# Performance work log

Measured on AMD Instinct MI355X. Metric: run time of the kernel, lower is better.

Reference implementation:

```python
import jax, jax.numpy as jnp
import numpy as np

N_NODES = 50000
N_EDGES = 800000
IN_DIM = 128
HIDDEN = 128
NUM_CLASSES = 2
NUM_GRAPHS = 512


def _linear_params(key, fan_in, fan_out):
    # torch nn.Linear default init: U(-1/sqrt(fan_in), 1/sqrt(fan_in))
    k1, k2 = jax.random.split(key)
    bound = 1.0 / np.sqrt(fan_in)
    W = jax.random.uniform(k1, (fan_in, fan_out), jnp.float32, -bound, bound)
    b = jax.random.uniform(k2, (fan_out,), jnp.float32, -bound, bound)
    return W, b


def setup_inputs() -> dict:
    key = jax.random.key(0)
    ks = jax.random.split(key, 8)
    x = jax.random.normal(ks[0], (N_NODES, IN_DIM), jnp.float32)
    edge_index = jax.random.randint(ks[1], (2, N_EDGES), 0, N_NODES, jnp.int64)
    batch = jnp.sort(jax.random.randint(ks[2], (N_NODES,), 0, NUM_GRAPHS, jnp.int64))
    W1a, b1a = _linear_params(ks[3], IN_DIM, HIDDEN)
    W1b, b1b = _linear_params(ks[4], HIDDEN, HIDDEN)
    W2a, b2a = _linear_params(ks[5], HIDDEN, HIDDEN)
    W2b, b2b = _linear_params(ks[6], HIDDEN, HIDDEN)
    Wfc, bfc = _linear_params(ks[7], HIDDEN, NUM_CLASSES)
    return {"x": x, "edge_index": edge_index, "batch": batch,
            "W1a": W1a, "b1a": b1a, "W1b": W1b, "b1b": b1b,
            "W2a": W2a, "b2a": b2a, "W2b": W2b, "b2b": b2b,
            "Wfc": Wfc, "bfc": bfc}


def _gin_layer(x, src, dst, Wa, ba, Wb, bb):
    # GINConv (eps=0): h_i = MLP(x_i + sum_{j->i} x_j)
    agg = jax.ops.segment_sum(x[src], dst, num_segments=N_NODES)
    h = x + agg
    h = jax.nn.relu(h @ Wa + ba)
    h = h @ Wb + bb
    return jax.nn.relu(h)  # outer F.relu in forward; dropout is identity (eval)


def reference(x, edge_index, batch, W1a, b1a, W1b, b1b, W2a, b2a, W2b, b2b, Wfc, bfc):
    src, dst = edge_index[0], edge_index[1]
    h = _gin_layer(x, src, dst, W1a, b1a, W1b, b1b)
    h = _gin_layer(h, src, dst, W2a, b2a, W2b, b2b)
    # global mean pool per graph
    sums = jax.ops.segment_sum(h, batch, num_segments=NUM_GRAPHS)
    counts = jax.ops.segment_sum(jnp.ones((N_NODES,), h.dtype), batch, num_segments=NUM_GRAPHS)
    g_emb = sums / jnp.maximum(counts, 1.0)[:, None]
    return g_emb @ Wfc + bfc  # [NUM_GRAPHS, NUM_CLASSES]
```

## Files before the change

### kernel.cpp

```cpp
#include <hip/hip_runtime.h>

typedef unsigned short ushort_t;
typedef unsigned int uint_t;

typedef __bf16 bf16x8 __attribute__((ext_vector_type(8)));
typedef float f32x4 __attribute__((ext_vector_type(4)));

#define N_NODES 50000
#define N_EDGES 800000
#define DIM 128
#define NUM_GRAPHS 512
#define LDA 136

#define ELL_CAP 64

#define NBUCK 256
#define BUCK_SZ 196
#define FIFO_CAP 4096
#define A_CHUNK 2048
#define A_BLOCKS ((N_EDGES + A_CHUNK - 1) / A_CHUNK)

#define PREP_X_BLOCKS 6250
#define PREP_W_BLOCKS 256
#define PREP_B_BLOCKS 196
#define PREP_TOTAL (A_BLOCKS + PREP_X_BLOCKS + PREP_W_BLOCKS + PREP_B_BLOCKS + 1)

__device__ __forceinline__ float bf2f(ushort_t u) {
    return __uint_as_float(((uint_t)u) << 16);
}
__device__ __forceinline__ ushort_t f2bf(float f) {
    uint_t u = __float_as_uint(f);
    u = (u + 0x7FFF + ((u >> 16) & 1)) >> 16;
    return (ushort_t)u;
}
__device__ __forceinline__ bf16x8 as_bf16x8(uint4 v) {
    return __builtin_bit_cast(bf16x8, v);
}

__global__ void zero_detect_kernel(int* gcnt, const void* xraw,
                                   const void* eiraw, int* flags) {
    int i = threadIdx.x;
    if (i < NBUCK) gcnt[i] = 0;
    if (i == 0) {
        const ushort_t* u = (const ushort_t*)xraw;
        int extreme = 0;
        for (int k = 0; k < 128; ++k) {
            int e = (u[k] >> 7) & 0xFF;
            if (e >= 0xC0) extreme++;
        }
        flags[0] = (extreme > 8) ? 1 : 0;
        const int* p = (const int*)eiraw;
        int nonzero = 0;
        for (int k = 1; k < 64; k += 2) nonzero += (p[k] != 0);
        flags[1] = (nonzero == 0) ? 1 : 0;
    }
}

__global__ __launch_bounds__(256) void prep_all_kernel(
    const void* xraw, const void* braw, const void* eiraw,
    const void* W0, const void* W1, const void* W2, const void* W3,
    const void* pb1a, const void* pb1b, const void* pb2a, const void* pb2b,
    const void* pWfc, const void* pbfc, const int* __restrict__ flags,
    ushort_t* __restrict__ xout, ushort_t* __restrict__ wpout,
    int* __restrict__ batch32, float* __restrict__ params,
    int* __restrict__ gcnt, uint_t* __restrict__ fifo) {
    __shared__ int lcnt[NBUCK];
    __shared__ int lbase[NBUCK];
    int b = blockIdx.x;
    int tid = threadIdx.x;
    if (b < A_BLOCKS) {
        lcnt[tid] = 0;
        __syncthreads();
        const int* p = (const int*)eiraw;
        int i64 = flags[1];
        int base_e = b * A_CHUNK;
        int gk[8], rk[8];
        uint_t pk[8];
#pragma unroll
        for (int k = 0; k < 8; ++k) {
            int e = base_e + k * 256 + tid;
            int valid = e < N_EDGES;
            int s = 0, d = 0;
            if (valid) {
                if (i64) { s = p[2 * e]; d = p[2 * (N_EDGES + e)]; }
                else     { s = p[e];     d = p[N_EDGES + e]; }
            }
            int g = d / BUCK_SZ;
            gk[k] = valid ? g : -1;
            pk[k] = (uint_t)s | ((uint_t)(d - g * BUCK_SZ) << 16);
            rk[k] = valid ? atomicAdd(&lcnt[g], 1) : 0;
        }
        __syncthreads();
        lbase[tid] = atomicAdd(&gcnt[tid], lcnt[tid]);
        __syncthreads();
#pragma unroll
        for (int k = 0; k < 8; ++k) {
            if (gk[k] >= 0) {
                int pos = lbase[gk[k]] + rk[k];
                if (pos < FIFO_CAP)
                    fifo[(size_t)gk[k] * FIFO_CAP + pos] = pk[k];
            }
        }
    } else if (b < A_BLOCKS + PREP_X_BLOCKS) {
        if (flags[0]) {
            int i = (b - A_BLOCKS) * 256 + tid;
            if (i < N_NODES * DIM / 4) {
                float4 v = ((const float4*)xraw)[i];
                ushort4 o;
                o.x = f2bf(v.x); o.y = f2bf(v.y); o.z = f2bf(v.z); o.w = f2bf(v.w);
                ((ushort4*)xout)[i] = o;
            }
        }
    } else if (b < A_BLOCKS + PREP_X_BLOCKS + PREP_W_BLOCKS) {
        int gidx = (b - A_BLOCKS - PREP_X_BLOCKS) * 256 + tid;
        int which = gidx >> 14;
        const void* W = (which == 0) ? W0 : (which == 1) ? W1 : (which == 2) ? W2 : W3;
        int idx = gidx & 16383;
        int j = idx & 7;
        int L = (idx >> 3) & 63;
        int t = (idx >> 9) & 7;
        int s = idx >> 12;
        int k = s * 32 + (L >> 4) * 8 + j;
        int n = t * 16 + (L & 15);
        int off = k * DIM + n;
        wpout[gidx] = flags[0] ? f2bf(((const float*)W)[off]) : ((const ushort_t*)W)[off];
    } else if (b < A_BLOCKS + PREP_X_BLOCKS + PREP_W_BLOCKS + PREP_B_BLOCKS) {
        int i = (b - A_BLOCKS - PREP_X_BLOCKS - PREP_W_BLOCKS) * 256 + tid;
        if (i < N_NODES) {
            const int* p = (const int*)braw;
            batch32[i] = flags[1] ? p[2 * i] : p[i];
        }
    } else {
        for (int i = tid; i < 770; i += 256) {
            const void* srcp;
            int j;
            if (i < 128)      { srcp = pb1a; j = i; }
            else if (i < 256) { srcp = pb1b; j = i - 128; }
            else if (i < 384) { srcp = pb2a; j = i - 256; }
            else if (i < 512) { srcp = pb2b; j = i - 384; }
            else if (i < 768) { srcp = pWfc; j = i - 512; }
            else              { srcp = pbfc; j = i - 768; }
            params[i] = flags[0] ? ((const float*)srcp)[j] : bf2f(((const ushort_t*)srcp)[j]);
        }
    }
}

__global__ __launch_bounds__(256) void scatter_kernel(const uint_t* __restrict__ fifo,
                                                      const int* __restrict__ gcnt,
                                                      int* __restrict__ cnt,
                                                      ushort_t* __restrict__ ell,
                                                      float* __restrict__ gsum) {
    __shared__ int lcnt[BUCK_SZ];
    int b = blockIdx.x;
    int tid = threadIdx.x;
    gsum[b * 256 + tid] = 0.f;
    if (tid < BUCK_SZ) lcnt[tid] = 0;
    __syncthreads();
    int n = gcnt[b];
    if (n > FIFO_CAP) n = FIFO_CAP;
    const uint_t* f = fifo + (size_t)b * FIFO_CAP;
    int node0 = b * BUCK_SZ;
    for (int i = tid; i < n; i += 256) {
        uint_t e = f[i];
        int dl = (int)(e >> 16);
        int slot = atomicAdd(&lcnt[dl], 1);
        if (slot < ELL_CAP)
            ell[(size_t)(node0 + dl) * ELL_CAP + slot] = (ushort_t)(e & 0xFFFFu);
    }
    __syncthreads();
    if (tid < BUCK_SZ) {
        int node = node0 + tid;
        if (node < N_NODES) {
            int deg = lcnt[tid];
            cnt[node] = (deg > ELL_CAP) ? ELL_CAP : deg;
        }
    }
}

__global__ __launch_bounds__(256) void agg_kernel(const ushort_t* __restrict__ featA,
                                                  const void* __restrict__ featB,
                                                  const int* __restrict__ flags,
                                                  const int* __restrict__ deg,
                                                  const ushort_t* __restrict__ ell,
                                                  ushort_t* __restrict__ hout) {
    int n = blockIdx.x * 16 + (threadIdx.x >> 4);
    int lane = threadIdx.x & 15;
    if (n >= N_NODES) return;
    const ushort_t* feat = featA;
    if (flags && !flags[0]) feat = (const ushort_t*)featB;
    const uint4* fp = reinterpret_cast<const uint4*>(feat);
    uint4 v = fp[(size_t)n * 16 + lane];
    float a0 = bf2f((ushort_t)(v.x & 0xffff));
    float a1 = bf2f((ushort_t)(v.x >> 16));
    float a2 = bf2f((ushort_t)(v.y & 0xffff));
    float a3 = bf2f((ushort_t)(v.y >> 16));
    float a4 = bf2f((ushort_t)(v.z & 0xffff));
    float a5 = bf2f((ushort_t)(v.z >> 16));
    float a6 = bf2f((ushort_t)(v.w & 0xffff));
    float a7 = bf2f((ushort_t)(v.w >> 16));
    int e1 = deg[n];
    const uint4* __restrict__ rp4 = reinterpret_cast<const uint4*>(ell + (size_t)n * ELL_CAP);
    const ushort_t* __restrict__ row = ell + (size_t)n * ELL_CAP;
    int j = 0;
#define ACC8(V) \
    a0 += bf2f((ushort_t)((V).x & 0xffff)); a1 += bf2f((ushort_t)((V).x >> 16)); \
    a2 += bf2f((ushort_t)((V).y & 0xffff)); a3 += bf2f((ushort_t)((V).y >> 16)); \
    a4 += bf2f((ushort_t)((V).z & 0xffff)); a5 += bf2f((ushort_t)((V).z >> 16)); \
    a6 += bf2f((ushort_t)((V).w & 0xffff)); a7 += bf2f((ushort_t)((V).w >> 16));
    for (; j + 8 <= e1; j += 8) {
        uint4 ra = rp4[j >> 3];
        int s0 = (int)(ra.x & 0xffff), s1 = (int)(ra.x >> 16);
        int s2 = (int)(ra.y & 0xffff), s3 = (int)(ra.y >> 16);
        int s4 = (int)(ra.z & 0xffff), s5 = (int)(ra.z >> 16);
        int s6 = (int)(ra.w & 0xffff), s7 = (int)(ra.w >> 16);
        uint4 g0 = fp[(size_t)s0 * 16 + lane];
        uint4 g1 = fp[(size_t)s1 * 16 + lane];
        uint4 g2 = fp[(size_t)s2 * 16 + lane];
        uint4 g3 = fp[(size_t)s3 * 16 + lane];
        uint4 g4 = fp[(size_t)s4 * 16 + lane];
        uint4 g5 = fp[(size_t)s5 * 16 + lane];
        uint4 g6 = fp[(size_t)s6 * 16 + lane];
        uint4 g7 = fp[(size_t)s7 * 16 + lane];
        ACC8(g0) ACC8(g1) ACC8(g2) ACC8(g3)
        ACC8(g4) ACC8(g5) ACC8(g6) ACC8(g7)
    }
    if (j + 4 <= e1) {
        uint2 ra = *reinterpret_cast<const uint2*>(row + j);
        int s0 = (int)(ra.x & 0xffff), s1 = (int)(ra.x >> 16);
        int s2 = (int)(ra.y & 0xffff), s3 = (int)(ra.y >> 16);
        uint4 g0 = fp[(size_t)s0 * 16 + lane];
        uint4 g1 = fp[(size_t)s1 * 16 + lane];
        uint4 g2 = fp[(size_t)s2 * 16 + lane];
        uint4 g3 = fp[(size_t)s3 * 16 + lane];
        ACC8(g0) ACC8(g1) ACC8(g2) ACC8(g3)
        j += 4;
    }
    for (; j < e1; ++j) {
        int s = (int)row[j];
        uint4 g0 = fp[(size_t)s * 16 + lane];
        ACC8(g0)
    }
#undef ACC8
    uint4 o;
    o.x = (uint_t)f2bf(a0) | ((uint_t)f2bf(a1) << 16);
    o.y = (uint_t)f2bf(a2) | ((uint_t)f2bf(a3) << 16);
    o.z = (uint_t)f2bf(a4) | ((uint_t)f2bf(a5) << 16);
    o.w = (uint_t)f2bf(a6) | ((uint_t)f2bf(a7) << 16);
    reinterpret_cast<uint4*>(hout)[(size_t)n * 16 + lane] = o;
}

__global__ __launch_bounds__(256) void mlp_kernel(const ushort_t* __restrict__ hin,
                                                  const ushort_t* __restrict__ wpA,
                                                  const float* __restrict__ ba,
                                                  const ushort_t* __restrict__ wpB,
                                                  const float* __restrict__ bb,
                                                  ushort_t* __restrict__ hout) {
    __shared__ ushort_t As[64 * LDA];
    int tid = threadIdx.x;
    int wave = tid >> 6;
    int lane = tid & 63;
    int quad = lane >> 4;
    int cl = lane & 15;
    int row0 = blockIdx.x * 64;

    bf16x8 B1[2][4], B2[2][4];
#pragma unroll
    for (int ti = 0; ti < 2; ++ti) {
        int t = 2 * wave + ti;
#pragma unroll
        for (int s = 0; s < 4; ++s) {
            B1[ti][s] = as_bf16x8(reinterpret_cast<const uint4*>(wpA)[(s * 8 + t) * 64 + lane]);
            B2[ti][s] = as_bf16x8(reinterpret_cast<const uint4*>(wpB)[(s * 8 + t) * 64 + lane]);
        }
    }

    for (int i = tid; i < 64 * 16; i += 256) {
        int r = i >> 4, c8 = i & 15;
        uint4 v = make_uint4(0u, 0u, 0u, 0u);
        int gr = row0 + r;
        if (gr < N_NODES)
            v = reinterpret_cast<const uint4*>(hin + (size_t)gr * DIM)[c8];
        *reinterpret_cast<uint4*>(&As[r * LDA + c8 * 8]) = v;
    }
    __syncthreads();

    f32x4 acc[4][2];
#pragma unroll
    for (int m = 0; m < 4; ++m)
#pragma unroll
        for (int ti = 0; ti < 2; ++ti)
#pragma unroll
            for (int r = 0; r < 4; ++r) acc[m][ti][r] = 0.f;

#pragma unroll
    for (int s = 0; s < 4; ++s) {
#pragma unroll
        for (int m = 0; m < 4; ++m) {
            bf16x8 a = *reinterpret_cast<const bf16x8*>(&As[(m * 16 + cl) * LDA + s * 32 + quad * 8]);
#pragma unroll
            for (int ti = 0; ti < 2; ++ti)
                acc[m][ti] = __builtin_amdgcn_mfma_f32_16x16x32_bf16(a, B1[ti][s], acc[m][ti], 0, 0, 0);
        }
    }
    __syncthreads();

#pragma unroll
    for (int ti = 0; ti < 2; ++ti) {
        int col = 32 * wave + ti * 16 + cl;
        float bv = ba[col];
#pragma unroll
        for (int m = 0; m < 4; ++m)
#pragma unroll
            for (int r = 0; r < 4; ++r) {
                float v = acc[m][ti][r] + bv;
                As[(m * 16 + quad * 4 + r) * LDA + col] = f2bf(fmaxf(v, 0.f));
            }
    }
    __syncthreads();

#pragma unroll
    for (int m = 0; m < 4; ++m)
#pragma unroll
        for (int ti = 0; ti < 2; ++ti)
#pragma unroll
            for (int r = 0; r < 4; ++r) acc[m][ti][r] = 0.f;

#pragma unroll
    for (int s = 0; s < 4; ++s) {
#pragma unroll
        for (int m = 0; m < 4; ++m) {
            bf16x8 a = *reinterpret_cast<const bf16x8*>(&As[(m * 16 + cl) * LDA + s * 32 + quad * 8]);
#pragma unroll
            for (int ti = 0; ti < 2; ++ti)
                acc[m][ti] = __builtin_amdgcn_mfma_f32_16x16x32_bf16(a, B2[ti][s], acc[m][ti], 0, 0, 0);
        }
    }

#pragma unroll
    for (int ti = 0; ti < 2; ++ti) {
        int col = 32 * wave + ti * 16 + cl;
        float bv = bb[col];
#pragma unroll
        for (int m = 0; m < 4; ++m)
#pragma unroll
            for (int r = 0; r < 4; ++r) {
                int gr = row0 + m * 16 + quad * 4 + r;
                if (gr < N_NODES) {
                    float v = acc[m][ti][r] + bv;
                    hout[(size_t)gr * DIM + col] = f2bf(fmaxf(v, 0.f));
                }
            }
    }
}

__global__ __launch_bounds__(256) void mlp_pool_kernel(const ushort_t* __restrict__ hin,
                                                       const ushort_t* __restrict__ wpA,
                                                       const float* __restrict__ ba,
                                                       const ushort_t* __restrict__ wpB,
                                                       const float* __restrict__ bb,
                                                       const int* __restrict__ batch32,
                                                       float* __restrict__ gsum) {
    __shared__ ushort_t As[64 * LDA];
    int tid = threadIdx.x;
    int wave = tid >> 6;
    int lane = tid & 63;
    int quad = lane >> 4;
    int cl = lane & 15;
    int row0 = blockIdx.x * 64;

    bf16x8 B1[2][4], B2[2][4];
#pragma unroll
    for (int ti = 0; ti < 2; ++ti) {
        int t = 2 * wave + ti;
#pragma unroll
        for (int s = 0; s < 4; ++s) {
            B1[ti][s] = as_bf16x8(reinterpret_cast<const uint4*>(wpA)[(s * 8 + t) * 64 + lane]);
            B2[ti][s] = as_bf16x8(reinterpret_cast<const uint4*>(wpB)[(s * 8 + t) * 64 + lane]);
        }
    }

    for (int i = tid; i < 64 * 16; i += 256) {
        int r = i >> 4, c8 = i & 15;
        uint4 v = make_uint4(0u, 0u, 0u, 0u);
        int gr = row0 + r;
        if (gr < N_NODES)
            v = reinterpret_cast<const uint4*>(hin + (size_t)gr * DIM)[c8];
        *reinterpret_cast<uint4*>(&As[r * LDA + c8 * 8]) = v;
    }
    __syncthreads();

    f32x4 acc[4][2];
#pragma unroll
    for (int m = 0; m < 4; ++m)
#pragma unroll
        for (int ti = 0; ti < 2; ++ti)
#pragma unroll
            for (int r = 0; r < 4; ++r) acc[m][ti][r] = 0.f;

#pragma unroll
    for (int s = 0; s < 4; ++s) {
#pragma unroll
        for (int m = 0; m < 4; ++m) {
            bf16x8 a = *reinterpret_cast<const bf16x8*>(&As[(m * 16 + cl) * LDA + s * 32 + quad * 8]);
#pragma unroll
            for (int ti = 0; ti < 2; ++ti)
                acc[m][ti] = __builtin_amdgcn_mfma_f32_16x16x32_bf16(a, B1[ti][s], acc[m][ti], 0, 0, 0);
        }
    }
    __syncthreads();

#pragma unroll
    for (int ti = 0; ti < 2; ++ti) {
        int col = 32 * wave + ti * 16 + cl;
        float bv = ba[col];
#pragma unroll
        for (int m = 0; m < 4; ++m)
#pragma unroll
            for (int r = 0; r < 4; ++r) {
                float v = acc[m][ti][r] + bv;
                As[(m * 16 + quad * 4 + r) * LDA + col] = f2bf(fmaxf(v, 0.f));
            }
    }
    __syncthreads();

#pragma unroll
    for (int m = 0; m < 4; ++m)
#pragma unroll
        for (int ti = 0; ti < 2; ++ti)
#pragma unroll
            for (int r = 0; r < 4; ++r) acc[m][ti][r] = 0.f;

#pragma unroll
    for (int s = 0; s < 4; ++s) {
#pragma unroll
        for (int m = 0; m < 4; ++m) {
            bf16x8 a = *reinterpret_cast<const bf16x8*>(&As[(m * 16 + cl) * LDA + s * 32 + quad * 8]);
#pragma unroll
            for (int ti = 0; ti < 2; ++ti)
                acc[m][ti] = __builtin_amdgcn_mfma_f32_16x16x32_bf16(a, B2[ti][s], acc[m][ti], 0, 0, 0);
        }
    }
    __syncthreads();

#pragma unroll
    for (int ti = 0; ti < 2; ++ti) {
        int col = 32 * wave + ti * 16 + cl;
        float bv = bb[col];
#pragma unroll
        for (int m = 0; m < 4; ++m)
#pragma unroll
            for (int r = 0; r < 4; ++r) {
                float v = acc[m][ti][r] + bv;
                As[(m * 16 + quad * 4 + r) * LDA + col] = f2bf(fmaxf(v, 0.f));
            }
    }
    __syncthreads();

    int c = tid & 127;
    int rbase = (tid >> 7) * 32;
    float accp = 0.f;
    int curg = -1;
    for (int r = rbase; r < rbase + 32; ++r) {
        int gr = row0 + r;
        if (gr >= N_NODES) break;
        int g = batch32[gr];
        if (g != curg) {
            if (curg >= 0) atomicAdd(&gsum[curg * DIM + c], accp);
            curg = g;
            accp = 0.f;
        }
        accp += bf2f(As[r * LDA + c]);
    }
    if (curg >= 0) atomicAdd(&gsum[curg * DIM + c], accp);
}

__global__ __launch_bounds__(64) void fc_kernel(const float* __restrict__ gsum,
                                                const int* __restrict__ batch,
                                                const float* __restrict__ params,
                                                const int* __restrict__ flags,
                                                void* __restrict__ out) {
    int g = blockIdx.x;
    int l = threadIdx.x;
    int lo = 0, hi = N_NODES;
    while (lo < hi) { int mid = (lo + hi) >> 1; if (batch[mid] < g) lo = mid + 1; else hi = mid; }
    int start = lo;
    hi = N_NODES;
    while (lo < hi) { int mid = (lo + hi) >> 1; if (batch[mid] < g + 1) lo = mid + 1; else hi = mid; }
    int cnt = lo - start;
    float inv = 1.0f / (float)(cnt > 0 ? cnt : 1);
    float m0 = gsum[g * DIM + l] * inv;
    float m1 = gsum[g * DIM + 64 + l] * inv;
    float p0 = m0 * params[512 + l * 2 + 0] + m1 * params[512 + (64 + l) * 2 + 0];
    float p1 = m0 * params[512 + l * 2 + 1] + m1 * params[512 + (64 + l) * 2 + 1];
#pragma unroll
    for (int off = 32; off > 0; off >>= 1) {
        p0 += __shfl_down(p0, off, 64);
        p1 += __shfl_down(p1, off, 64);
    }
    if (l == 0) {
        float o0 = p0 + params[768];
        float o1 = p1 + params[769];
        if (flags[0]) {
            ((float*)out)[g * 2 + 0] = o0;
            ((float*)out)[g * 2 + 1] = o1;
        } else {
            ((ushort_t*)out)[g * 2 + 0] = f2bf(o0);
            ((ushort_t*)out)[g * 2 + 1] = f2bf(o1);
        }
    }
}

extern "C" void kernel_launch(void* const* d_in, const int* in_sizes, int n_in,
                              void* d_out, int out_size, void* d_ws, size_t ws_size,
                              hipStream_t stream) {
    const void* x = d_in[0];
    const void* ei = d_in[1];
    const void* batch = d_in[2];
    const void* W1a = d_in[3];
    const void* b1a = d_in[4];
    const void* W1b = d_in[5];
    const void* b1b = d_in[6];
    const void* W2a = d_in[7];
    const void* b2a = d_in[8];
    const void* W2b = d_in[9];
    const void* b2b = d_in[10];
    const void* Wfc = d_in[11];
    const void* bfc = d_in[12];

    char* base = (char*)d_ws;
    ushort_t* hX = (ushort_t*)base;   base += (size_t)N_NODES * DIM * 2;
    ushort_t* hA = (ushort_t*)base;   base += (size_t)N_NODES * DIM * 2;
    ushort_t* ell = (ushort_t*)base;  base += (size_t)N_NODES * ELL_CAP * 2;
    uint_t* fifo = (uint_t*)base;     base += (size_t)NBUCK * FIFO_CAP * 4;
    int* cnt = (int*)base;            base += (size_t)N_NODES * 4;
    int* batch32 = (int*)base;        base += (size_t)N_NODES * 4;
    int* gcnt = (int*)base;           base += NBUCK * 4;
    ushort_t* wp = (ushort_t*)base;   base += 4 * 16384 * 2;
    float* params = (float*)base;     base += 772 * 4;
    float* gsum = (float*)base;       base += (size_t)NUM_GRAPHS * DIM * 4;
    int* flags = (int*)base;          base += 16;

    ushort_t* wpA1 = wp;
    ushort_t* wpB1 = wp + 16384;
    ushort_t* wpA2 = wp + 2 * 16384;
    ushort_t* wpB2 = wp + 3 * 16384;

    zero_detect_kernel<<<1, 256, 0, stream>>>(gcnt, x, ei, flags);
    prep_all_kernel<<<PREP_TOTAL, 256, 0, stream>>>(x, batch, ei, W1a, W1b, W2a, W2b,
                                                    b1a, b1b, b2a, b2b, Wfc, bfc, flags,
                                                    hX, wp, batch32, params, gcnt, fifo);
    scatter_kernel<<<NBUCK, 256, 0, stream>>>(fifo, gcnt, cnt, ell, gsum);

    agg_kernel<<<(N_NODES + 15) / 16, 256, 0, stream>>>(hX, x, flags, cnt, ell, hA);
    mlp_kernel<<<(N_NODES + 63) / 64, 256, 0, stream>>>(hA, wpA1, params + 0, wpB1, params + 128, hA);
    agg_kernel<<<(N_NODES + 15) / 16, 256, 0, stream>>>(hA, hA, nullptr, cnt, ell, hX);
    mlp_pool_kernel<<<(N_NODES + 63) / 64, 256, 0, stream>>>(hX, wpA2, params + 256, wpB2, params + 384,
                                                             batch32, gsum);
    fc_kernel<<<NUM_GRAPHS, 64, 0, stream>>>(gsum, batch32, params, flags, d_out);
}
```

Before: 226.9 us.

## Fuse GIN pipeline into a single cooperative persistent kernel with grid syncs

Replaces the chain of eight kernel launches with one cooperative persistent kernel that loops over virtual blocks for each stage and separates stages with grid-wide syncs. Flag detection moves into each block, which skips the x-conversion blocks when x is already bf16. Zeroing of gsum and gcnt moves to a memset, and the MLP now loads the second weight set after the first GEMM to lower register pressure. This removes launch gaps and inter-kernel drain, but grid.sync costs and a persistent grid capped at 1536 blocks may hurt load balance in the irregular aggregation stages.

```diff
diff --git a/kernel.cpp b/kernel.cpp
--- a/kernel.cpp
+++ b/kernel.cpp
@@ -1,4 +1,7 @@
 #include <hip/hip_runtime.h>
+#include <hip/hip_cooperative_groups.h>
+
+namespace cg = cooperative_groups;
 
 typedef unsigned short ushort_t;
 typedef unsigned int uint_t;
@@ -25,6 +28,12 @@
 #define PREP_B_BLOCKS 196
 #define PREP_TOTAL (A_BLOCKS + PREP_X_BLOCKS + PREP_W_BLOCKS + PREP_B_BLOCKS + 1)
 
+#define AGG_VBLOCKS ((N_NODES + 15) / 16)
+#define MLP_VBLOCKS ((N_NODES + 63) / 64)
+#define FC_VBLOCKS (NUM_GRAPHS / 4)
+
+#define SMEM_BYTES (64 * LDA * 2)
+
 __device__ __forceinline__ float bf2f(ushort_t u) {
     return __uint_as_float(((uint_t)u) << 16);
 }
@@ -37,42 +46,35 @@
     return __builtin_bit_cast(bf16x8, v);
 }
 
-__global__ void zero_detect_kernel(int* gcnt, const void* xraw,
-                                   const void* eiraw, int* flags) {
-    int i = threadIdx.x;
-    if (i < NBUCK) gcnt[i] = 0;
-    if (i == 0) {
-        const ushort_t* u = (const ushort_t*)xraw;
-        int extreme = 0;
-        for (int k = 0; k < 128; ++k) {
-            int e = (u[k] >> 7) & 0xFF;
-            if (e >= 0xC0) extreme++;
-        }
-        flags[0] = (extreme > 8) ? 1 : 0;
-        const int* p = (const int*)eiraw;
-        int nonzero = 0;
-        for (int k = 1; k < 64; k += 2) nonzero += (p[k] != 0);
-        flags[1] = (nonzero == 0) ? 1 : 0;
-    }
-}
-
-__global__ __launch_bounds__(256) void prep_all_kernel(
+__device__ __forceinline__ void detect_flags(const void* xraw, const void* eiraw,
+                                             int* f32f, int* i64f) {
+    const ushort_t* u = (const ushort_t*)xraw;
+    int extreme = 0;
+    for (int k = 0; k < 128; ++k) {
+        int e = (u[k] >> 7) & 0xFF;
+        if (e >= 0xC0) extreme++;
+    }
+    *f32f = (extreme > 8) ? 1 : 0;
+    const int* p = (const int*)eiraw;
+    int nonzero = 0;
+    for (int k = 1; k < 64; k += 2) nonzero += (p[k] != 0);
+    *i64f = (nonzero == 0) ? 1 : 0;
+}
+
+__device__ __forceinline__ void dev_prep(
+    int b, int tid, char* smemc,
     const void* xraw, const void* braw, const void* eiraw,
     const void* W0, const void* W1, const void* W2, const void* W3,
     const void* pb1a, const void* pb1b, const void* pb2a, const void* pb2b,
-    const void* pWfc, const void* pbfc, const int* __restrict__ flags,
-    ushort_t* __restrict__ xout, ushort_t* __restrict__ wpout,
-    int* __restrict__ batch32, float* __restrict__ params,
-    int* __restrict__ gcnt, uint_t* __restrict__ fifo) {
-    __shared__ int lcnt[NBUCK];
-    __shared__ int lbase[NBUCK];
-    int b = blockIdx.x;
-    int tid = threadIdx.x;
+    const void* pWfc, const void* pbfc, int f32f, int i64f, int xblocks,
+    ushort_t* xout, ushort_t* wpout, int* batch32, float* params,
+    int* gcnt, uint_t* fifo) {
+    int* lcnt = (int*)smemc;
+    int* lbase = lcnt + NBUCK;
     if (b < A_BLOCKS) {
         lcnt[tid] = 0;
         __syncthreads();
         const int* p = (const int*)eiraw;
-        int i64 = flags[1];
         int base_e = b * A_CHUNK;
         int gk[8], rk[8];
         uint_t pk[8];
@@ -82,8 +84,8 @@
             int valid = e < N_EDGES;
             int s = 0, d = 0;
             if (valid) {
-                if (i64) { s = p[2 * e]; d = p[2 * (N_EDGES + e)]; }
-                else     { s = p[e];     d = p[N_EDGES + e]; }
+                if (i64f) { s = p[2 * e]; d = p[2 * (N_EDGES + e)]; }
+                else      { s = p[e];     d = p[N_EDGES + e]; }
             }
             int g = d / BUCK_SZ;
             gk[k] = valid ? g : -1;
@@ -101,8 +103,8 @@
                     fifo[(size_t)gk[k] * FIFO_CAP + pos] = pk[k];
             }
         }
-    } else if (b < A_BLOCKS + PREP_X_BLOCKS) {
-        if (flags[0]) {
+    } else if (b < A_BLOCKS + xblocks) {
+        if (f32f) {
             int i = (b - A_BLOCKS) * 256 + tid;
             if (i < N_NODES * DIM / 4) {
                 float4 v = ((const float4*)xraw)[i];
@@ -111,8 +113,8 @@
                 ((ushort4*)xout)[i] = o;
             }
         }
-    } else if (b < A_BLOCKS + PREP_X_BLOCKS + PREP_W_BLOCKS) {
-        int gidx = (b - A_BLOCKS - PREP_X_BLOCKS) * 256 + tid;
+    } else if (b < A_BLOCKS + xblocks + PREP_W_BLOCKS) {
+        int gidx = (b - A_BLOCKS - xblocks) * 256 + tid;
         int which = gidx >> 14;
         const void* W = (which == 0) ? W0 : (which == 1) ? W1 : (which == 2) ? W2 : W3;
         int idx = gidx & 16383;
@@ -123,12 +125,12 @@
         int k = s * 32 + (L >> 4) * 8 + j;
         int n = t * 16 + (L & 15);
         int off = k * DIM + n;
-        wpout[gidx] = flags[0] ? f2bf(((const float*)W)[off]) : ((const ushort_t*)W)[off];
-    } else if (b < A_BLOCKS + PREP_X_BLOCKS + PREP_W_BLOCKS + PREP_B_BLOCKS) {
-        int i = (b - A_BLOCKS - PREP_X_BLOCKS - PREP_W_BLOCKS) * 256 + tid;
+        wpout[gidx] = f32f ? f2bf(((const float*)W)[off]) : ((const ushort_t*)W)[off];
+    } else if (b < A_BLOCKS + xblocks + PREP_W_BLOCKS + PREP_B_BLOCKS) {
+        int i = (b - A_BLOCKS - xblocks - PREP_W_BLOCKS) * 256 + tid;
         if (i < N_NODES) {
             const int* p = (const int*)braw;
-            batch32[i] = flags[1] ? p[2 * i] : p[i];
+            batch32[i] = i64f ? p[2 * i] : p[i];
         }
     } else {
         for (int i = tid; i < 770; i += 256) {
@@ -140,20 +142,15 @@
             else if (i < 512) { srcp = pb2b; j = i - 384; }
             else if (i < 768) { srcp = pWfc; j = i - 512; }
             else              { srcp = pbfc; j = i - 768; }
-            params[i] = flags[0] ? ((const float*)srcp)[j] : bf2f(((const ushort_t*)srcp)[j]);
-        }
-    }
-}
-
-__global__ __launch_bounds__(256) void scatter_kernel(const uint_t* __restrict__ fifo,
-                                                      const int* __restrict__ gcnt,
-                                                      int* __restrict__ cnt,
-                                                      ushort_t* __restrict__ ell,
-                                                      float* __restrict__ gsum) {
-    __shared__ int lcnt[BUCK_SZ];
-    int b = blockIdx.x;
-    int tid = threadIdx.x;
-    gsum[b * 256 + tid] = 0.f;
+            params[i] = f32f ? ((const float*)srcp)[j] : bf2f(((const ushort_t*)srcp)[j]);
+        }
+    }
+}
+
+__device__ __forceinline__ void dev_scatter(int b, int tid, char* smemc,
+                                            const uint_t* fifo, const int* gcnt,
+                                            int* cnt, ushort_t* ell) {
+    int* lcnt = (int*)smemc;
     if (tid < BUCK_SZ) lcnt[tid] = 0;
     __syncthreads();
     int n = gcnt[b];
@@ -177,17 +174,12 @@
     }
 }
 
-__global__ __launch_bounds__(256) void agg_kernel(const ushort_t* __restrict__ featA,
-                                                  const void* __restrict__ featB,
-                                                  const int* __restrict__ flags,
-                                                  const int* __restrict__ deg,
-                                                  const ushort_t* __restrict__ ell,
-                                                  ushort_t* __restrict__ hout) {
-    int n = blockIdx.x * 16 + (threadIdx.x >> 4);
-    int lane = threadIdx.x & 15;
+__device__ __forceinline__ void dev_agg(int b, int tid, const ushort_t* feat,
+                                        const int* deg, const ushort_t* ell,
+                                        ushort_t* hout) {
+    int n = b * 16 + (tid >> 4);
+    int lane = tid & 15;
     if (n >= N_NODES) return;
-    const ushort_t* feat = featA;
-    if (flags && !flags[0]) feat = (const ushort_t*)featB;
     const uint4* fp = reinterpret_cast<const uint4*>(feat);
     uint4 v = fp[(size_t)n * 16 + lane];
     float a0 = bf2f((ushort_t)(v.x & 0xffff));
@@ -199,8 +191,8 @@
     float a6 = bf2f((ushort_t)(v.w & 0xffff));
     float a7 = bf2f((ushort_t)(v.w >> 16));
     int e1 = deg[n];
-    const uint4* __restrict__ rp4 = reinterpret_cast<const uint4*>(ell + (size_t)n * ELL_CAP);
-    const ushort_t* __restrict__ row = ell + (size_t)n * ELL_CAP;
+    const uint4* rp4 = reinterpret_cast<const uint4*>(ell + (size_t)n * ELL_CAP);
+    const ushort_t* row = ell + (size_t)n * ELL_CAP;
     int j = 0;
 #define ACC8(V) \
     a0 += bf2f((ushort_t)((V).x & 0xffff)); a1 += bf2f((ushort_t)((V).x >> 16)); \
@@ -249,31 +241,21 @@
     reinterpret_cast<uint4*>(hout)[(size_t)n * 16 + lane] = o;
 }
 
-__global__ __launch_bounds__(256) void mlp_kernel(const ushort_t* __restrict__ hin,
-                                                  const ushort_t* __restrict__ wpA,
-                                                  const float* __restrict__ ba,
-                                                  const ushort_t* __restrict__ wpB,
-                                                  const float* __restrict__ bb,
-                                                  ushort_t* __restrict__ hout) {
-    __shared__ ushort_t As[64 * LDA];
-    int tid = threadIdx.x;
-    int wave = tid >> 6;
-    int lane = tid & 63;
-    int quad = lane >> 4;
-    int cl = lane & 15;
-    int row0 = blockIdx.x * 64;
-
-    bf16x8 B1[2][4], B2[2][4];
+__device__ __forceinline__ void dev_mlp(int b, int tid, char* smemc,
+                                        const ushort_t* hin, const ushort_t* wpA,
+                                        const float* ba, const ushort_t* wpB,
+                                        const float* bb, ushort_t* hout) {
+    ushort_t* As = (ushort_t*)smemc;
+    int wave = tid >> 6, lane = tid & 63, quad = lane >> 4, cl = lane & 15;
+    int row0 = b * 64;
+    bf16x8 B[2][4];
 #pragma unroll
     for (int ti = 0; ti < 2; ++ti) {
         int t = 2 * wave + ti;
 #pragma unroll
-        for (int s = 0; s < 4; ++s) {
-            B1[ti][s] = as_bf16x8(reinterpret_cast<const uint4*>(wpA)[(s * 8 + t) * 64 + lane]);
-            B2[ti][s] = as_bf16x8(reinterpret_cast<const uint4*>(wpB)[(s * 8 + t) * 64 + lane]);
-        }
-    }
-
+        for (int s = 0; s < 4; ++s)
+            B[ti][s] = as_bf16x8(reinterpret_cast<const uint4*>(wpA)[(s * 8 + t) * 64 + lane]);
+    }
     for (int i = tid; i < 64 * 16; i += 256) {
         int r = i >> 4, c8 = i & 15;
         uint4 v = make_uint4(0u, 0u, 0u, 0u);
@@ -283,7 +265,6 @@
         *reinterpret_cast<uint4*>(&As[r * LDA + c8 * 8]) = v;
     }
     __syncthreads();
-
     f32x4 acc[4][2];
 #pragma unroll
     for (int m = 0; m < 4; ++m)
@@ -291,19 +272,16 @@
         for (int ti = 0; ti < 2; ++ti)
 #pragma unroll
             for (int r = 0; r < 4; ++r) acc[m][ti][r] = 0.f;
-
-#pragma unroll
-    for (int s = 0; s < 4; ++s) {
+#pragma unroll
+    for (int s = 0; s < 4; ++s)
 #pragma unroll
         for (int m = 0; m < 4; ++m) {
             bf16x8 a = *reinterpret_cast<const bf16x8*>(&As[(m * 16 + cl) * LDA + s * 32 + quad * 8]);
 #pragma unroll
             for (int ti = 0; ti < 2; ++ti)
-                acc[m][ti] = __builtin_amdgcn_mfma_f32_16x16x32_bf16(a, B1[ti][s], acc[m][ti], 0, 0, 0);
-        }
-    }
-    __syncthreads();
-
+                acc[m][ti] = __builtin_amdgcn_mfma_f32_16x16x32_bf16(a, B[ti][s], acc[m][ti], 0, 0, 0);
+        }
+    __syncthreads();
 #pragma unroll
     for (int ti = 0; ti < 2; ++ti) {
         int col = 32 * wave + ti * 16 + cl;
@@ -317,25 +295,28 @@
             }
     }
     __syncthreads();
-
+#pragma unroll
+    for (int ti = 0; ti < 2; ++ti) {
+        int t = 2 * wave + ti;
+#pragma unroll
+        for (int s = 0; s < 4; ++s)
+            B[ti][s] = as_bf16x8(reinterpret_cast<const uint4*>(wpB)[(s * 8 + t) * 64 + lane]);
+    }
 #pragma unroll
     for (int m = 0; m < 4; ++m)
 #pragma unroll
         for (int ti = 0; ti < 2; ++ti)
 #pragma unroll
             for (int r = 0; r < 4; ++r) acc[m][ti][r] = 0.f;
-
-#pragma unroll
-    for (int s = 0; s < 4; ++s) {
+#pragma unroll
+    for (int s = 0; s < 4; ++s)
 #pragma unroll
         for (int m = 0; m < 4; ++m) {
             bf16x8 a = *reinterpret_cast<const bf16x8*>(&As[(m * 16 + cl) * LDA + s * 32 + quad * 8]);
 #pragma unroll
             for (int ti = 0; ti < 2; ++ti)
-                acc[m][ti] = __builtin_amdgcn_mfma_f32_16x16x32_bf16(a, B2[ti][s], acc[m][ti], 0, 0, 0);
-        }
-    }
-
+                acc[m][ti] = __builtin_amdgcn_mfma_f32_16x16x32_bf16(a, B[ti][s], acc[m][ti], 0, 0, 0);
+        }
 #pragma unroll
     for (int ti = 0; ti < 2; ++ti) {
         int col = 32 * wave + ti * 16 + cl;
@@ -351,34 +332,25 @@
                 }
             }
     }
-}
-
-__global__ __launch_bounds__(256) void mlp_pool_kernel(const ushort_t* __restrict__ hin,
-                                                       const ushort_t* __restrict__ wpA,
-                                                       const float* __restrict__ ba,
-                                                       const ushort_t* __restrict__ wpB,
-                                                       const float* __restrict__ bb,
-                                                       const int* __restrict__ batch32,
-                                                       float* __restrict__ gsum) {
-    __shared__ ushort_t As[64 * LDA];
-    int tid = threadIdx.x;
-    int wave = tid >> 6;
-    int lane = tid & 63;
-    int quad = lane >> 4;
-    int cl = lane & 15;
-    int row0 = blockIdx.x * 64;
-
-    bf16x8 B1[2][4], B2[2][4];
+    __syncthreads();
+}
+
+__device__ __forceinline__ void dev_mlp_pool(int b, int tid, char* smemc,
+                                             const ushort_t* hin, const ushort_t* wpA,
+                                             const float* ba, const ushort_t* wpB,
+                                             const float* bb, const int* batch32,
+                                             float* gsum) {
+    ushort_t* As = (ushort_t*)smemc;
+    int wave = tid >> 6, lane = tid & 63, quad = lane >> 4, cl = lane & 15;
+    int row0 = b * 64;
+    bf16x8 B[2][4];
 #pragma unroll
     for (int ti = 0; ti < 2; ++ti) {
         int t = 2 * wave + ti;
 #pragma unroll
-        for (int s = 0; s < 4; ++s) {
-            B1[ti][s] = as_bf16x8(reinterpret_cast<const uint4*>(wpA)[(s * 8 + t) * 64 + lane]);
-            B2[ti][s] = as_bf16x8(reinterpret_cast<const uint4*>(wpB)[(s * 8 + t) * 64 + lane]);
-        }
-    }
-
+        for (int s = 0; s < 4; ++s)
+            B[ti][s] = as_bf16x8(reinterpret_cast<const uint4*>(wpA)[(s * 8 + t) * 64 + lane]);
+    }
     for (int i = tid; i < 64 * 16; i += 256) {
         int r = i >> 4, c8 = i & 15;
         uint4 v = make_uint4(0u, 0u, 0u, 0u);
@@ -388,7 +360,6 @@
         *reinterpret_cast<uint4*>(&As[r * LDA + c8 * 8]) = v;
     }
     __syncthreads();
-
     f32x4 acc[4][2];
 #pragma unroll
     for (int m = 0; m < 4; ++m)
@@ -396,19 +367,16 @@
         for (int ti = 0; ti < 2; ++ti)
 #pragma unroll
             for (int r = 0; r < 4; ++r) acc[m][ti][r] = 0.f;
-
-#pragma unroll
-    for (int s = 0; s < 4; ++s) {
+#pragma unroll
+    for (int s = 0; s < 4; ++s)
 #pragma unroll
         for (int m = 0; m < 4; ++m) {
             bf16x8 a = *reinterpret_cast<const bf16x8*>(&As[(m * 16 + cl) * LDA + s * 32 + quad * 8]);
 #pragma unroll
             for (int ti = 0; ti < 2; ++ti)
-                acc[m][ti] = __builtin_amdgcn_mfma_f32_16x16x32_bf16(a, B1[ti][s], acc[m][ti], 0, 0, 0);
-        }
-    }
-    __syncthreads();
-
+                acc[m][ti] = __builtin_amdgcn_mfma_f32_16x16x32_bf16(a, B[ti][s], acc[m][ti], 0, 0, 0);
+        }
+    __syncthreads();
 #pragma unroll
     for (int ti = 0; ti < 2; ++ti) {
         int col = 32 * wave + ti * 16 + cl;
@@ -422,26 +390,29 @@
             }
     }
     __syncthreads();
-
+#pragma unroll
+    for (int ti = 0; ti < 2; ++ti) {
+        int t = 2 * wave + ti;
+#pragma unroll
+        for (int s = 0; s < 4; ++s)
+            B[ti][s] = as_bf16x8(reinterpret_cast<const uint4*>(wpB)[(s * 8 + t) * 64 + lane]);
+    }
 #pragma unroll
     for (int m = 0; m < 4; ++m)
 #pragma unroll
         for (int ti = 0; ti < 2; ++ti)
 #pragma unroll
             for (int r = 0; r < 4; ++r) acc[m][ti][r] = 0.f;
-
-#pragma unroll
-    for (int s = 0; s < 4; ++s) {
+#pragma unroll
+    for (int s = 0; s < 4; ++s)
 #pragma unroll
         for (int m = 0; m < 4; ++m) {
             bf16x8 a = *reinterpret_cast<const bf16x8*>(&As[(m * 16 + cl) * LDA + s * 32 + quad * 8]);
 #pragma unroll
             for (int ti = 0; ti < 2; ++ti)
-                acc[m][ti] = __builtin_amdgcn_mfma_f32_16x16x32_bf16(a, B2[ti][s], acc[m][ti], 0, 0, 0);
-        }
-    }
-    __syncthreads();
-
+                acc[m][ti] = __builtin_amdgcn_mfma_f32_16x16x32_bf16(a, B[ti][s], acc[m][ti], 0, 0, 0);
+        }
+    __syncthreads();
 #pragma unroll
     for (int ti = 0; ti < 2; ++ti) {
         int col = 32 * wave + ti * 16 + cl;
@@ -455,7 +426,6 @@
             }
     }
     __syncthreads();
-
     int c = tid & 127;
     int rbase = (tid >> 7) * 32;
     float accp = 0.f;
@@ -472,15 +442,15 @@
         accp += bf2f(As[r * LDA + c]);
     }
     if (curg >= 0) atomicAdd(&gsum[curg * DIM + c], accp);
-}
-
-__global__ __launch_bounds__(64) void fc_kernel(const float* __restrict__ gsum,
-                                                const int* __restrict__ batch,
-                                                const float* __restrict__ params,
-                                                const int* __restrict__ flags,
-                                                void* __restrict__ out) {
-    int g = blockIdx.x;
-    int l = threadIdx.x;
+    __syncthreads();
+}
+
+__device__ __forceinline__ void dev_fc(int vb, int tid, const float* gsum,
+                                       const int* batch, const float* params,
+                                       int outf32, void* out) {
+    int wave = tid >> 6, l = tid & 63;
+    int g = vb * 4 + wave;
+    if (g >= NUM_GRAPHS) return;
     int lo = 0, hi = N_NODES;
     while (lo < hi) { int mid = (lo + hi) >> 1; if (batch[mid] < g) lo = mid + 1; else hi = mid; }
     int start = lo;
@@ -500,7 +470,7 @@
     if (l == 0) {
         float o0 = p0 + params[768];
         float o1 = p1 + params[769];
-        if (flags[0]) {
+        if (outf32) {
             ((float*)out)[g * 2 + 0] = o0;
             ((float*)out)[g * 2 + 1] = o1;
         } else {
@@ -508,6 +478,113 @@
             ((ushort_t*)out)[g * 2 + 1] = f2bf(o1);
         }
     }
+}
+
+struct MegaArgs {
+    const void *x, *ei, *batch;
+    const void *W1a, *b1a, *W1b, *b1b, *W2a, *b2a, *W2b, *b2b, *Wfc, *bfc;
+    ushort_t *hX, *hA, *ell;
+    uint_t *fifo;
+    int *cnt, *batch32, *gcnt;
+    ushort_t *wp;
+    float *params, *gsum;
+    void *out;
+};
+
+__global__ __launch_bounds__(256, 6) void mega_kernel(MegaArgs a) {
+    cg::grid_group grid = cg::this_grid();
+    __shared__ __align__(16) char smem[SMEM_BYTES];
+    __shared__ int sflags[2];
+    int tid = threadIdx.x;
+    if (tid == 0) detect_flags(a.x, a.ei, &sflags[0], &sflags[1]);
+    __syncthreads();
+    int f32f = sflags[0], i64f = sflags[1];
+    int nblk = gridDim.x, bid = blockIdx.x;
+
+    int xblocks = f32f ? PREP_X_BLOCKS : 0;
+    int ptotal = A_BLOCKS + xblocks + PREP_W_BLOCKS + PREP_B_BLOCKS + 1;
+    for (int vb = bid; vb < ptotal; vb += nblk)
+        dev_prep(vb, tid, smem, a.x, a.batch, a.ei, a.W1a, a.W1b, a.W2a, a.W2b,
+                 a.b1a, a.b1b, a.b2a, a.b2b, a.Wfc, a.bfc, f32f, i64f, xblocks,
+                 a.hX, a.wp, a.batch32, a.params, a.gcnt, a.fifo);
+    grid.sync();
+    for (int vb = bid; vb < NBUCK; vb += nblk)
+        dev_scatter(vb, tid, smem, a.fifo, a.gcnt, a.cnt, a.ell);
+    grid.sync();
+    const ushort_t* feat0 = f32f ? a.hX : (const ushort_t*)a.x;
+    for (int vb = bid; vb < AGG_VBLOCKS; vb += nblk)
+        dev_agg(vb, tid, feat0, a.cnt, a.ell, a.hA);
+    grid.sync();
+    for (int vb = bid; vb < MLP_VBLOCKS; vb += nblk)
+        dev_mlp(vb, tid, smem, a.hA, a.wp, a.params + 0, a.wp + 16384,
+                a.params + 128, a.hA);
+    grid.sync();
+    for (int vb = bid; vb < AGG_VBLOCKS; vb += nblk)
+        dev_agg(vb, tid, a.hA, a.cnt, a.ell, a.hX);
+    grid.sync();
+    for (int vb = bid; vb < MLP_VBLOCKS; vb += nblk)
+        dev_mlp_pool(vb, tid, smem, a.hX, a.wp + 2 * 16384, a.params + 256,
+                     a.wp + 3 * 16384, a.params + 384, a.batch32, a.gsum);
+    grid.sync();
+    for (int vb = bid; vb < FC_VBLOCKS; vb += nblk)
+        dev_fc(vb, tid, a.gsum, a.batch32, a.params, f32f, a.out);
+}
+
+__global__ void flags_kernel(const void* xraw, const void* eiraw, int* flags) {
+    if (threadIdx.x == 0) detect_flags(xraw, eiraw, &flags[0], &flags[1]);
+}
+
+__global__ __launch_bounds__(256) void prep_all_kernel(
+    const void* xraw, const void* braw, const void* eiraw,
+    const void* W0, const void* W1, const void* W2, const void* W3,
+    const void* pb1a, const void* pb1b, const void* pb2a, const void* pb2b,
+    const void* pWfc, const void* pbfc, const int* __restrict__ flags,
+    ushort_t* xout, ushort_t* wpout, int* batch32, float* params,
+    int* gcnt, uint_t* fifo) {
+    __shared__ __align__(16) char smem[NBUCK * 8];
+    dev_prep(blockIdx.x, threadIdx.x, smem, xraw, braw, eiraw, W0, W1, W2, W3,
+             pb1a, pb1b, pb2a, pb2b, pWfc, pbfc, flags[0], flags[1],
+             PREP_X_BLOCKS, xout, wpout, batch32, params, gcnt, fifo);
+}
+
+__global__ __launch_bounds__(256) void scatter_kernel(const uint_t* fifo,
+                                                      const int* gcnt, int* cnt,
+                                                      ushort_t* ell) {
+    __shared__ __align__(16) char smem[BUCK_SZ * 4];
+    dev_scatter(blockIdx.x, threadIdx.x, smem, fifo, gcnt, cnt, ell);
+}
+
+__global__ __launch_bounds__(256) void agg_kernel(const ushort_t* featA,
+                                                  const void* featB,
+                                                  const int* flags,
+                                                  const int* deg,
+                                                  const ushort_t* ell,
+                                                  ushort_t* hout) {
+    const ushort_t* feat = featA;
+    if (flags && !flags[0]) feat = (const ushort_t*)featB;
+    dev_agg(blockIdx.x, threadIdx.x, feat, deg, ell, hout);
+}
+
+__global__ __launch_bounds__(256) void mlp_kernel(const ushort_t* hin,
+                                                  const ushort_t* wpA, const float* ba,
+                                                  const ushort_t* wpB, const float* bb,
+                                                  ushort_t* hout) {
+    __shared__ __align__(16) char smem[SMEM_BYTES];
+    dev_mlp(blockIdx.x, threadIdx.x, smem, hin, wpA, ba, wpB, bb, hout);
+}
+
+__global__ __launch_bounds__(256) void mlp_pool_kernel(const ushort_t* hin,
+                                                       const ushort_t* wpA, const float* ba,
+                                                       const ushort_t* wpB, const float* bb,
+                                                       const int* batch32, float* gsum) {
+    __shared__ __align__(16) char smem[SMEM_BYTES];
+    dev_mlp_pool(blockIdx.x, threadIdx.x, smem, hin, wpA, ba, wpB, bb, batch32, gsum);
+}
+
+__global__ __launch_bounds__(256) void fc_kernel(const float* gsum, const int* batch,
+                                                 const float* params, const int* flags,
+                                                 void* out) {
+    dev_fc(blockIdx.x, threadIdx.x, gsum, batch, params, flags[0], out);
 }
 
 extern "C" void kernel_launch(void* const* d_in, const int* in_sizes, int n_in,
@@ -534,10 +611,10 @@
     uint_t* fifo = (uint_t*)base;     base += (size_t)NBUCK * FIFO_CAP * 4;
     int* cnt = (int*)base;            base += (size_t)N_NODES * 4;
     int* batch32 = (int*)base;        base += (size_t)N_NODES * 4;
-    int* gcnt = (int*)base;           base += NBUCK * 4;
     ushort_t* wp = (ushort_t*)base;   base += 4 * 16384 * 2;
     float* params = (float*)base;     base += 772 * 4;
     float* gsum = (float*)base;       base += (size_t)NUM_GRAPHS * DIM * 4;
+    int* gcnt = (int*)base;           base += NBUCK * 4;
     int* flags = (int*)base;          base += 16;
 
     ushort_t* wpA1 = wp;
@@ -545,16 +622,48 @@
     ushort_t* wpA2 = wp + 2 * 16384;
     ushort_t* wpB2 = wp + 3 * 16384;
 
-    zero_detect_kernel<<<1, 256, 0, stream>>>(gcnt, x, ei, flags);
-    prep_all_kernel<<<PREP_TOTAL, 256, 0, stream>>>(x, batch, ei, W1a, W1b, W2a, W2b,
-                                                    b1a, b1b, b2a, b2b, Wfc, bfc, flags,
-                                                    hX, wp, batch32, params, gcnt, fifo);
-    scatter_kernel<<<NBUCK, 256, 0, stream>>>(fifo, gcnt, cnt, ell, gsum);
-
-    agg_kernel<<<(N_NODES + 15) / 16, 256, 0, stream>>>(hX, x, flags, cnt, ell, hA);
-    mlp_kernel<<<(N_NODES + 63) / 64, 256, 0, stream>>>(hA, wpA1, params + 0, wpB1, params + 128, hA);
-    agg_kernel<<<(N_NODES + 15) / 16, 256, 0, stream>>>(hA, hA, nullptr, cnt, ell, hX);
-    mlp_pool_kernel<<<(N_NODES + 63) / 64, 256, 0, stream>>>(hX, wpA2, params + 256, wpB2, params + 384,
-                                                             batch32, gsum);
-    fc_kernel<<<NUM_GRAPHS, 64, 0, stream>>>(gsum, batch32, params, flags, d_out);
-}
+    hipMemsetAsync(gsum, 0, (size_t)NUM_GRAPHS * DIM * 4 + NBUCK * 4, stream);
+
+    MegaArgs ma;
+    ma.x = x; ma.ei = ei; ma.batch = batch;
+    ma.W1a = W1a; ma.b1a = b1a; ma.W1b = W1b; ma.b1b = b1b;
+    ma.W2a = W2a; ma.b2a = b2a; ma.W2b = W2b; ma.b2b = b2b;
+    ma.Wfc = Wfc; ma.bfc = bfc;
+    ma.hX = hX; ma.hA = hA; ma.ell = ell; ma.fifo = fifo;
+    ma.cnt = cnt; ma.batch32 = batch32; ma.gcnt = gcnt;
+    ma.wp = wp; ma.params = params; ma.gsum = gsum; ma.out = d_out;
+    void* kargs[] = { &ma };
+
+    static int s_cus = 0;
+    if (s_cus == 0) {
+        hipDeviceProp_t p;
+        if (hipGetDeviceProperties(&p, 0) == hipSuccess && p.multiProcessorCount > 0)
+            s_cus = p.multiProcessorCount;
+        else
+            s_cus = 256;
+    }
+    int occ = 0;
+    hipError_t oerr = hipOccupancyMaxActiveBlocksPerMultiprocessor(&occ, mega_kernel, 256, 0);
+    bool coop_ok = false;
+    if (oerr == hipSuccess && occ >= 1) {
+        int grid = occ * s_cus;
+        if (grid > 1536) grid = 1536;
+        hipError_t lerr = hipLaunchCooperativeKernel((const void*)mega_kernel,
+                                                     dim3(grid), dim3(256), kargs, 0, stream);
+        coop_ok = (lerr == hipSuccess);
+        if (!coop_ok) (void)hipGetLastError();
+    }
+    if (!coop_ok) {
+        flags_kernel<<<1, 64, 0, stream>>>(x, ei, flags);
+        prep_all_kernel<<<PREP_TOTAL, 256, 0, stream>>>(x, batch, ei, W1a, W1b, W2a, W2b,
+                                                        b1a, b1b, b2a, b2b, Wfc, bfc, flags,
+                                                        hX, wp, batch32, params, gcnt, fifo);
+        scatter_kernel<<<NBUCK, 256, 0, stream>>>(fifo, gcnt, cnt, ell);
+        agg_kernel<<<AGG_VBLOCKS, 256, 0, stream>>>(hX, x, flags, cnt, ell, hA);
+        mlp_kernel<<<MLP_VBLOCKS, 256, 0, stream>>>(hA, wpA1, params + 0, wpB1, params + 128, hA);
+        agg_kernel<<<AGG_VBLOCKS, 256, 0, stream>>>(hA, hA, nullptr, cnt, ell, hX);
+        mlp_pool_kernel<<<MLP_VBLOCKS, 256, 0, stream>>>(hX, wpA2, params + 256, wpB2, params + 384,
+                                                         batch32, gsum);
+        fc_kernel<<<FC_VBLOCKS, 256, 0, stream>>>(gsum, batch32, params, flags, d_out);
+    }
+}
```

Result: slower. 831.1 us (+266.3%).
